# Kernel optimization log

Hardware: AMD Instinct MI355X
Metric: run time of the kernel (lower is better)

The kernel has to match this reference:

```python
import jax, jax.numpy as jnp
import numpy as np

N_NODES = 50000
N_EDGES = 800000
D = 128
N_GRAPHS = 64
EPS = 1e-5


def _bn(x, g, b):
    # BatchNorm1d training-mode statistics over the node/graph axis
    mu = x.mean(axis=0)
    var = x.var(axis=0)
    return g * (x - mu) / jnp.sqrt(var + EPS) + b


def setup_inputs() -> dict:
    key = jax.random.key(0)
    ks = jax.random.split(key, 32)
    s = 0.05
    inp = {
        'x': jax.random.normal(ks[0], (N_NODES, D), dtype=jnp.float32),
        'edge_index': jax.random.randint(ks[1], (2, N_EDGES), 0, N_NODES, dtype=jnp.int32),
        'batch': jnp.sort(jax.random.randint(ks[2], (N_NODES,), 0, N_GRAPHS, dtype=jnp.int32)),
        # stacked ResGatedGraphConv params for 3 layers (key/query/value/skip)
        'Wk': jax.random.normal(ks[3], (3, D, D)) * s,
        'bk': jnp.zeros((3, D)),
        'Wq': jax.random.normal(ks[4], (3, D, D)) * s,
        'bq': jnp.zeros((3, D)),
        'Wv': jax.random.normal(ks[5], (3, D, D)) * s,
        'bv': jnp.zeros((3, D)),
        'Ws': jax.random.normal(ks[6], (3, D, D)) * s,
        'bs': jnp.zeros((3, D)),
        # per-layer conv BatchNorm affine params
        'g_cl': jnp.ones((3, D)), 'b_cl': jnp.zeros((3, D)),
        # pool norms
        'g_gap': jnp.ones((D,)), 'b_gap': jnp.zeros((D,)),
        'g_gsp': jnp.ones((D,)), 'b_gsp': jnp.zeros((D,)),
        # MLP head: 2*D -> 256 -> 128 -> 5
        'W1': jax.random.normal(ks[7], (2 * D, 256)) * s, 'b1': jnp.zeros((256,)),
        'g1': jnp.ones((256,)), 'bt1': jnp.zeros((256,)),
        'W2': jax.random.normal(ks[8], (256, 128)) * s, 'b2': jnp.zeros((128,)),
        'g2': jnp.ones((128,)), 'bt2': jnp.zeros((128,)),
        'Wl': jax.random.normal(ks[9], (128, 5)) * s, 'bl': jnp.zeros((5,)),
    }
    return inp


def reference(x, edge_index, batch, Wk, bk, Wq, bq, Wv, bv, Ws, bs, g_cl, b_cl,
              g_gap, b_gap, g_gsp, b_gsp, W1, b1, g1, bt1, W2, b2, g2, bt2, Wl, bl):
    src, dst = edge_index[0], edge_index[1]
    n = x.shape[0]
    for i in range(3):
        k = x @ Wk[i] + bk[i]   # target-side gate term
        q = x @ Wq[i] + bq[i]   # source-side gate term
        v = x @ Wv[i] + bv[i]   # messages
        gate = jax.nn.sigmoid(k[dst] + q[src])          # [E, D]
        agg = jax.ops.segment_sum(gate * v[src], dst, num_segments=n)
        x = agg + x @ Ws[i] + bs[i]                      # residual skip
        x = jax.nn.relu(x)
        x = _bn(x, g_cl[i], b_cl[i])
        # dropout: identity in eval mode
    counts = jax.ops.segment_sum(jnp.ones((n,), x.dtype), batch, num_segments=N_GRAPHS)
    gap = jax.ops.segment_sum(x, batch, num_segments=N_GRAPHS) / jnp.maximum(counts, 1.0)[:, None]
    gsp = jax.ops.segment_max(x, batch, num_segments=N_GRAPHS)
    gsp = jnp.where(counts[:, None] > 0, gsp, 0.0)
    gap = _bn(gap, g_gap, b_gap)
    gsp = _bn(gsp, g_gsp, b_gsp)
    out = jnp.concatenate([gap, gsp], axis=1)            # [G, 2D]
    out = _bn(jax.nn.relu(out @ W1 + b1), g1, bt1)
    out = _bn(jax.nn.relu(out @ W2 + b2), g2, bt2)
    return out @ Wl + bl                                  # [G, 5]
```

## Files before the change

### kernel.cpp

```cpp
#include <hip/hip_runtime.h>
#include <math.h>

#define N_NODES 50000
#define N_PAD 50048
#define N_EDGES 800000
#define D 128
#define N_GRAPHS 64
#define EPS 1e-5f
#define PCHUNK 16
#define GSTRIPES 8
#define SCAN_NB 196

typedef __attribute__((ext_vector_type(8))) short bf16x8;
typedef __attribute__((ext_vector_type(4))) float f32x4;
typedef __attribute__((ext_vector_type(2))) _Float16 h16x2;

static inline size_t align256(size_t x) { return (x + 255) & ~(size_t)255; }

__device__ inline unsigned short f2bf(float x) {
    unsigned u = __builtin_bit_cast(unsigned, x);
    u += 0x7FFFu + ((u >> 16) & 1u);
    return (unsigned short)(u >> 16);
}
__device__ inline float bf2f(unsigned short h) {
    unsigned u = (unsigned)h << 16;
    return __builtin_bit_cast(float, u);
}
__device__ inline unsigned short f2h(float x) {
    _Float16 h = (_Float16)x;
    return __builtin_bit_cast(unsigned short, h);
}

__device__ inline float fsigmoid(float z) {
    return __builtin_amdgcn_rcpf(1.0f + __expf(-z));
}

__global__ void prep_w(const float* __restrict__ Wk, const float* __restrict__ Wq,
                       const float* __restrict__ Wv, const float* __restrict__ Ws,
                       unsigned short* __restrict__ Whi, unsigned short* __restrict__ Wlo)
{
    const int j = blockIdx.x & 127;
    const int mat = (blockIdx.x >> 7) & 3;
    const int layer = blockIdx.x >> 9;
    const int k = threadIdx.x;
    const float* Wsrc = (mat == 0) ? Wk : (mat == 1) ? Wq : (mat == 2) ? Wv : Ws;
    const float w = Wsrc[((size_t)layer * D + k) * D + j];
    const unsigned short hi = f2bf(w);
    const unsigned short lo = f2bf(w - bf2f(hi));
    const size_t o = (((size_t)layer * 4 + mat) * D + j) * D + k;
    Whi[o] = hi;
    Wlo[o] = lo;
}

__global__ void convert_split(const float* __restrict__ X,
                              unsigned short* __restrict__ Xhi, unsigned short* __restrict__ Xlo)
{
    const size_t idx = (size_t)blockIdx.x * blockDim.x + threadIdx.x;
    if (idx >= (size_t)N_PAD * (D / 4)) return;
    const size_t n = idx >> 5;
    float4 v = make_float4(0.f, 0.f, 0.f, 0.f);
    if (n < N_NODES) v = ((const float4*)X)[idx];
    float xv[4] = {v.x, v.y, v.z, v.w};
    unsigned short hi[4], lo[4];
    #pragma unroll
    for (int c = 0; c < 4; ++c) {
        hi[c] = f2bf(xv[c]);
        lo[c] = f2bf(xv[c] - bf2f(hi[c]));
    }
    ((ushort4*)Xhi)[idx] = make_ushort4(hi[0], hi[1], hi[2], hi[3]);
    ((ushort4*)Xlo)[idx] = make_ushort4(lo[0], lo[1], lo[2], lo[3]);
}

__global__ void gemm_kqvs_mfma(
    const unsigned short* __restrict__ Xhi, const unsigned short* __restrict__ Xlo,
    const unsigned short* __restrict__ Whi, const unsigned short* __restrict__ Wlo,
    const float* __restrict__ bk, const float* __restrict__ bq,
    const float* __restrict__ bv, const float* __restrict__ bs,
    float* __restrict__ Kb, unsigned short* __restrict__ QVh, float* __restrict__ Sb)
{
    const int tid = threadIdx.x;
    const int wave = tid >> 6;
    const int mat = wave >> 1;
    const int cq = (wave & 1) + 2 * blockIdx.y;
    const int lane = tid & 63;
    const int l16 = lane & 15;
    const int lhi = lane >> 4;

    const unsigned short* wh = Whi + (size_t)mat * D * D;
    const unsigned short* wl = Wlo + (size_t)mat * D * D;
    bf16x8 bh[2][4], bl[2][4];
    #pragma unroll
    for (int t2 = 0; t2 < 2; ++t2) {
        const int tc = (cq * 2 + t2) * 16 + l16;
        const size_t wb = (size_t)tc * D;
        #pragma unroll
        for (int c = 0; c < 4; ++c) {
            bh[t2][c] = *(const bf16x8*)(wh + wb + c * 32 + lhi * 8);
            bl[t2][c] = *(const bf16x8*)(wl + wb + c * 32 + lhi * 8);
        }
    }

    const float* bb = (mat == 0) ? bk : (mat == 1) ? bq : (mat == 2) ? bv : bs;
    float bias[2];
    #pragma unroll
    for (int t2 = 0; t2 < 2; ++t2) bias[t2] = bb[(cq * 2 + t2) * 16 + l16];

    for (int s = 0; s < GSTRIPES; ++s) {
        const int r0 = (blockIdx.x * GSTRIPES + s) * 16;
        bf16x8 ah[4], al[4];
        const size_t arow = (size_t)(r0 + l16) * D;
        #pragma unroll
        for (int c = 0; c < 4; ++c) {
            ah[c] = *(const bf16x8*)(Xhi + arow + c * 32 + lhi * 8);
            al[c] = *(const bf16x8*)(Xlo + arow + c * 32 + lhi * 8);
        }
        f32x4 acc[2];
        acc[0] = (f32x4){0.f, 0.f, 0.f, 0.f};
        acc[1] = (f32x4){0.f, 0.f, 0.f, 0.f};
        #pragma unroll
        for (int t2 = 0; t2 < 2; ++t2) {
            #pragma unroll
            for (int c = 0; c < 4; ++c) {
                acc[t2] = __builtin_amdgcn_mfma_f32_16x16x32_bf16(ah[c], bh[t2][c], acc[t2], 0, 0, 0);
                acc[t2] = __builtin_amdgcn_mfma_f32_16x16x32_bf16(al[c], bh[t2][c], acc[t2], 0, 0, 0);
                acc[t2] = __builtin_amdgcn_mfma_f32_16x16x32_bf16(ah[c], bl[t2][c], acc[t2], 0, 0, 0);
            }
        }
        if (mat == 0 || mat == 3) {
            float* ob = (mat == 0) ? Kb : Sb;
            #pragma unroll
            for (int t2 = 0; t2 < 2; ++t2) {
                const int lc = (cq * 2 + t2) * 16 + l16;
                #pragma unroll
                for (int rgi = 0; rgi < 4; ++rgi) {
                    const int row = r0 + lhi * 4 + rgi;
                    if (row < N_NODES) ob[(size_t)row * D + lc] = acc[t2][rgi] + bias[t2];
                }
            }
        } else {
            unsigned short* base = QVh + ((mat == 2) ? 1 : 0);
            #pragma unroll
            for (int t2 = 0; t2 < 2; ++t2) {
                const int lc = (cq * 2 + t2) * 16 + l16;
                #pragma unroll
                for (int rgi = 0; rgi < 4; ++rgi) {
                    const int row = r0 + lhi * 4 + rgi;
                    if (row < N_NODES) base[2 * ((size_t)row * D + lc)] = f2h(acc[t2][rgi] + bias[t2]);
                }
            }
        }
    }
}

__global__ void hist_dst(const int* __restrict__ dst, int* __restrict__ cnt) {
    int e = blockIdx.x * blockDim.x + threadIdx.x;
    if (e < N_EDGES) atomicAdd(&cnt[dst[e]], 1);
}

__global__ void scan_block_sums(const int* __restrict__ cnt, int* __restrict__ bsum) {
    __shared__ int s[256];
    const int t = threadIdx.x;
    const int i = blockIdx.x * 256 + t;
    s[t] = (i < N_NODES) ? cnt[i] : 0;
    __syncthreads();
    #pragma unroll
    for (int off = 128; off > 0; off >>= 1) {
        if (t < off) s[t] += s[t + off];
        __syncthreads();
    }
    if (t == 0) bsum[blockIdx.x] = s[0];
}

__global__ void scan_block_offsets(const int* __restrict__ bsum, int* __restrict__ boff) {
    __shared__ int s[256];
    const int t = threadIdx.x;
    s[t] = (t < SCAN_NB) ? bsum[t] : 0;
    __syncthreads();
    for (int off = 1; off < 256; off <<= 1) {
        const int add = (t >= off) ? s[t - off] : 0;
        __syncthreads();
        s[t] += add;
        __syncthreads();
    }
    if (t < SCAN_NB) boff[t] = (t == 0) ? 0 : s[t - 1];
}

__global__ void scan_final(const int* __restrict__ cnt, const int* __restrict__ boff,
                           int* __restrict__ row_start, int* __restrict__ cursor) {
    __shared__ int s[256];
    const int t = threadIdx.x;
    const int i = blockIdx.x * 256 + t;
    const int v = (i < N_NODES) ? cnt[i] : 0;
    s[t] = v;
    __syncthreads();
    for (int off = 1; off < 256; off <<= 1) {
        const int add = (t >= off) ? s[t - off] : 0;
        __syncthreads();
        s[t] += add;
        __syncthreads();
    }
    if (i < N_NODES) {
        const int excl = boff[blockIdx.x] + s[t] - v;
        row_start[i] = excl;
        cursor[i] = excl;
    }
    if (i == N_NODES - 1) {
        row_start[N_NODES] = N_EDGES;
        cursor[N_NODES] = N_EDGES;
    }
}

__global__ void fill_csr(const int* __restrict__ src, const int* __restrict__ dst,
                         int* __restrict__ cursor, int* __restrict__ col) {
    int e = blockIdx.x * blockDim.x + threadIdx.x;
    if (e < N_EDGES) {
        int d = dst[e];
        int p = atomicAdd(&cursor[d], 1);
        col[p] = src[e];
    }
}

__global__ void aggregate(const float* __restrict__ Kb, const unsigned int* __restrict__ QV,
                          const float* __restrict__ Sb,
                          const int* __restrict__ row_start, const int* __restrict__ col,
                          float* __restrict__ H)
{
    const int tid = threadIdx.x;
    const int node = blockIdx.x * 2 + (tid >> 7);
    const int d = tid & 127;
    const float kd = Kb[(size_t)node * D + d];
    float acc = 0.f;
    const int e0 = row_start[node];
    const int e1 = row_start[node + 1];
    int e = e0;
    for (; e + 4 <= e1; e += 4) {
        const int s0 = col[e + 0];
        const int s1 = col[e + 1];
        const int s2 = col[e + 2];
        const int s3 = col[e + 3];
        const unsigned u0 = QV[(size_t)s0 * D + d];
        const unsigned u1 = QV[(size_t)s1 * D + d];
        const unsigned u2 = QV[(size_t)s2 * D + d];
        const unsigned u3 = QV[(size_t)s3 * D + d];
        const h16x2 a0 = __builtin_bit_cast(h16x2, u0);
        const h16x2 a1 = __builtin_bit_cast(h16x2, u1);
        const h16x2 a2 = __builtin_bit_cast(h16x2, u2);
        const h16x2 a3 = __builtin_bit_cast(h16x2, u3);
        acc = fmaf(fsigmoid(kd + (float)a0[0]), (float)a0[1], acc);
        acc = fmaf(fsigmoid(kd + (float)a1[0]), (float)a1[1], acc);
        acc = fmaf(fsigmoid(kd + (float)a2[0]), (float)a2[1], acc);
        acc = fmaf(fsigmoid(kd + (float)a3[0]), (float)a3[1], acc);
    }
    for (; e < e1; ++e) {
        const int s = col[e];
        const h16x2 a = __builtin_bit_cast(h16x2, QV[(size_t)s * D + d]);
        acc = fmaf(fsigmoid(kd + (float)a[0]), (float)a[1], acc);
    }
    H[(size_t)node * D + d] = fmaxf(acc + Sb[(size_t)node * D + d], 0.0f);
}

__global__ void bn_stats(const float* __restrict__ H, float* __restrict__ fsum,
                         float* __restrict__ fsq)
{
    __shared__ float s1[256], s2[256];
    const int tid = threadIdx.x;
    const int d = tid & 127;
    const int rowoff = tid >> 7;
    float sum = 0.f, sq = 0.f;
    for (int n = blockIdx.x * 2 + rowoff; n < N_NODES; n += gridDim.x * 2) {
        const float v = H[(size_t)n * D + d];
        sum += v; sq += v * v;
    }
    s1[tid] = sum; s2[tid] = sq;
    __syncthreads();
    if (tid < 128) {
        atomicAdd(&fsum[d], s1[tid] + s1[tid + 128]);
        atomicAdd(&fsq[d],  s2[tid] + s2[tid + 128]);
    }
}

__global__ void bn_apply(float* __restrict__ H, const float* __restrict__ fsum,
                         const float* __restrict__ fsq, const float* __restrict__ g,
                         const float* __restrict__ b)
{
    const int idx = blockIdx.x * blockDim.x + threadIdx.x;
    const int total = N_NODES * D / 4;
    if (idx >= total) return;
    float4 h = ((const float4*)H)[idx];
    float hv[4] = {h.x, h.y, h.z, h.w};
    const int dbase = (idx * 4) & 127;
    float o[4];
    #pragma unroll
    for (int c = 0; c < 4; ++c) {
        const int d = dbase + c;
        const float mu = fsum[d] * (1.0f / N_NODES);
        const float var = fsq[d] * (1.0f / N_NODES) - mu * mu;
        const float sc = g[d] * rsqrtf(var + EPS);
        o[c] = (hv[c] - mu) * sc + b[d];
    }
    ((float4*)H)[idx] = make_float4(o[0], o[1], o[2], o[3]);
}

__global__ void find_gstart(const int* __restrict__ batch, int* __restrict__ gstart) {
    const int g = threadIdx.x;
    if (g > N_GRAPHS) return;
    int lo = 0, hi = N_NODES;
    while (lo < hi) {
        int mid = (lo + hi) >> 1;
        if (batch[mid] < g) lo = mid + 1; else hi = mid;
    }
    gstart[g] = lo;
}

__global__ void pool_partial(const float* __restrict__ X, const int* __restrict__ gstart,
                             float* __restrict__ psum, float* __restrict__ pmax)
{
    const int g = blockIdx.x / PCHUNK;
    const int c = blockIdx.x % PCHUNK;
    const int d = threadIdx.x;
    const int lo = gstart[g], hi = gstart[g + 1];
    float sum = 0.f, mx = -INFINITY;
    for (int n = lo + c; n < hi; n += PCHUNK) {
        const float v = X[(size_t)n * D + d];
        sum += v;
        mx = fmaxf(mx, v);
    }
    psum[(size_t)blockIdx.x * D + d] = sum;
    pmax[(size_t)blockIdx.x * D + d] = mx;
}

__global__ void pool_combine(const float* __restrict__ psum, const float* __restrict__ pmax,
                             const int* __restrict__ gstart,
                             float* __restrict__ gap, float* __restrict__ gsp)
{
    const int g = blockIdx.x;
    const int d = threadIdx.x;
    float sum = 0.f, mx = -INFINITY;
    #pragma unroll
    for (int c = 0; c < PCHUNK; ++c) {
        sum += psum[(size_t)(g * PCHUNK + c) * D + d];
        mx = fmaxf(mx, pmax[(size_t)(g * PCHUNK + c) * D + d]);
    }
    const int cnt = gstart[g + 1] - gstart[g];
    gap[g * D + d] = sum / fmaxf((float)cnt, 1.0f);
    gsp[g * D + d] = (cnt > 0) ? mx : 0.0f;
}

__global__ void bn_rows(const float* __restrict__ A, int rows, int cols,
                        const float* __restrict__ g, const float* __restrict__ b,
                        float* __restrict__ out, int out_cols, int out_off)
{
    const int c = blockIdx.x * blockDim.x + threadIdx.x;
    if (c >= cols) return;
    float sum = 0.f, sq = 0.f;
    for (int r = 0; r < rows; ++r) {
        const float v = A[r * cols + c];
        sum += v; sq += v * v;
    }
    const float mu = sum / rows;
    const float var = sq / rows - mu * mu;
    const float sc = g[c] * rsqrtf(var + EPS);
    const float sh = b[c] - mu * sc;
    for (int r = 0; r < rows; ++r) {
        out[r * out_cols + out_off + c] = A[r * cols + c] * sc + sh;
    }
}

__global__ void gemm_small(const float* __restrict__ A, const float* __restrict__ W,
                           const float* __restrict__ bias, float* __restrict__ out,
                           int K, int C, int relu)
{
    __shared__ float as[256];
    const int r = blockIdx.x;
    for (int k = threadIdx.x; k < K; k += blockDim.x) as[k] = A[r * K + k];
    __syncthreads();
    const int j = threadIdx.x;
    if (j < C) {
        float acc = bias[j];
        for (int k = 0; k < K; ++k) acc = fmaf(as[k], W[k * C + j], acc);
        if (relu) acc = fmaxf(acc, 0.f);
        out[r * C + j] = acc;
    }
}

extern "C" void kernel_launch(void* const* d_in, const int* in_sizes, int n_in,
                              void* d_out, int out_size, void* d_ws, size_t ws_size,
                              hipStream_t stream)
{
    const float* x     = (const float*)d_in[0];
    const int*   ei    = (const int*)d_in[1];
    const int*   srcE  = ei;
    const int*   dstE  = ei + N_EDGES;
    const int*   batch = (const int*)d_in[2];
    const float* Wk = (const float*)d_in[3];  const float* bk = (const float*)d_in[4];
    const float* Wq = (const float*)d_in[5];  const float* bq = (const float*)d_in[6];
    const float* Wv = (const float*)d_in[7];  const float* bv = (const float*)d_in[8];
    const float* Ws = (const float*)d_in[9];  const float* bs = (const float*)d_in[10];
    const float* g_cl = (const float*)d_in[11]; const float* b_cl = (const float*)d_in[12];
    const float* g_gap = (const float*)d_in[13]; const float* b_gap = (const float*)d_in[14];
    const float* g_gsp = (const float*)d_in[15]; const float* b_gsp = (const float*)d_in[16];
    const float* W1 = (const float*)d_in[17]; const float* b1 = (const float*)d_in[18];
    const float* g1 = (const float*)d_in[19]; const float* bt1 = (const float*)d_in[20];
    const float* W2 = (const float*)d_in[21]; const float* b2 = (const float*)d_in[22];
    const float* g2 = (const float*)d_in[23]; const float* bt2 = (const float*)d_in[24];
    const float* Wl = (const float*)d_in[25]; const float* bl = (const float*)d_in[26];
    float* out = (float*)d_out;

    char* ws = (char*)d_ws;
    size_t off = 0;
    const size_t bufB = (size_t)N_NODES * D * sizeof(float);
    float* Kb = (float*)(ws + off); off = align256(off + bufB);
    unsigned short* QVh = (unsigned short*)(ws + off); off = align256(off + bufB);
    float* Sb = (float*)(ws + off); off = align256(off + bufB);
    float* H  = (float*)(ws + off); off = align256(off + bufB);
    unsigned short* Xhi = (unsigned short*)(ws + off); off = align256(off + (size_t)N_PAD * D * 2);
    unsigned short* Xlo = (unsigned short*)(ws + off); off = align256(off + (size_t)N_PAD * D * 2);
    unsigned short* Whi = (unsigned short*)(ws + off); off = align256(off + (size_t)12 * D * D * 2);
    unsigned short* Wlo = (unsigned short*)(ws + off); off = align256(off + (size_t)12 * D * D * 2);
    float* fsum = (float*)(ws + off); off = align256(off + 128 * sizeof(float));
    float* fsq  = (float*)(ws + off); off = align256(off + 128 * sizeof(float));
    int* cnt       = (int*)(ws + off); off = align256(off + (size_t)N_NODES * sizeof(int));
    int* row_start = (int*)(ws + off); off = align256(off + (size_t)(N_NODES + 1) * sizeof(int));
    int* cursor    = (int*)(ws + off); off = align256(off + (size_t)(N_NODES + 1) * sizeof(int));
    int* colI      = (int*)(ws + off); off = align256(off + (size_t)N_EDGES * sizeof(int));
    int* bsum      = (int*)(ws + off); off = align256(off + 256 * sizeof(int));
    int* boff      = (int*)(ws + off); off = align256(off + 256 * sizeof(int));
    int* gstart    = (int*)(ws + off); off = align256(off + (N_GRAPHS + 1) * sizeof(int));
    float* psum = (float*)(ws + off); off = align256(off + (size_t)N_GRAPHS * PCHUNK * D * sizeof(float));
    float* pmax = (float*)(ws + off); off = align256(off + (size_t)N_GRAPHS * PCHUNK * D * sizeof(float));
    float* gap = (float*)(ws + off); off = align256(off + (size_t)N_GRAPHS * D * sizeof(float));
    float* gsp = (float*)(ws + off); off = align256(off + (size_t)N_GRAPHS * D * sizeof(float));
    float* h0  = (float*)(ws + off); off = align256(off + (size_t)N_GRAPHS * 256 * sizeof(float));
    float* h1  = (float*)(ws + off); off = align256(off + (size_t)N_GRAPHS * 256 * sizeof(float));
    float* h2  = (float*)(ws + off); off = align256(off + (size_t)N_GRAPHS * 128 * sizeof(float));
    if (off > ws_size) return;

    hipMemsetAsync(cnt, 0, (size_t)N_NODES * sizeof(int), stream);
    hist_dst<<<(N_EDGES + 255) / 256, 256, 0, stream>>>(dstE, cnt);
    scan_block_sums<<<SCAN_NB, 256, 0, stream>>>(cnt, bsum);
    scan_block_offsets<<<1, 256, 0, stream>>>(bsum, boff);
    scan_final<<<SCAN_NB, 256, 0, stream>>>(cnt, boff, row_start, cursor);
    fill_csr<<<(N_EDGES + 255) / 256, 256, 0, stream>>>(srcE, dstE, cursor, colI);
    find_gstart<<<1, 128, 0, stream>>>(batch, gstart);
    prep_w<<<12 * 128, 128, 0, stream>>>(Wk, Wq, Wv, Ws, Whi, Wlo);
    convert_split<<<(N_PAD * (D / 4) + 255) / 256, 256, 0, stream>>>(x, Xhi, Xlo);

    for (int i = 0; i < 3; ++i) {
        gemm_kqvs_mfma<<<dim3(N_PAD / (16 * GSTRIPES), 2), 512, 0, stream>>>(
            Xhi, Xlo,
            Whi + (size_t)i * 4 * D * D, Wlo + (size_t)i * 4 * D * D,
            bk + i * D, bq + i * D, bv + i * D, bs + i * D,
            Kb, QVh, Sb);
        aggregate<<<N_NODES / 2, 256, 0, stream>>>(Kb, (const unsigned int*)QVh, Sb, row_start, colI, H);
        hipMemsetAsync(fsum, 0, 128 * sizeof(float), stream);
        hipMemsetAsync(fsq, 0, 128 * sizeof(float), stream);
        bn_stats<<<256, 256, 0, stream>>>(H, fsum, fsq);
        bn_apply<<<(N_NODES * D / 4 + 255) / 256, 256, 0, stream>>>(
            H, fsum, fsq, g_cl + i * D, b_cl + i * D);
        if (i < 2) {
            convert_split<<<(N_PAD * (D / 4) + 255) / 256, 256, 0, stream>>>(H, Xhi, Xlo);
        }
    }

    pool_partial<<<N_GRAPHS * PCHUNK, 128, 0, stream>>>(H, gstart, psum, pmax);
    pool_combine<<<N_GRAPHS, 128, 0, stream>>>(psum, pmax, gstart, gap, gsp);
    bn_rows<<<1, 128, 0, stream>>>(gap, N_GRAPHS, 128, g_gap, b_gap, h0, 256, 0);
    bn_rows<<<1, 128, 0, stream>>>(gsp, N_GRAPHS, 128, g_gsp, b_gsp, h0, 256, 128);

    gemm_small<<<N_GRAPHS, 256, 0, stream>>>(h0, W1, b1, h1, 256, 256, 1);
    bn_rows<<<1, 256, 0, stream>>>(h1, N_GRAPHS, 256, g1, bt1, h1, 256, 0);
    gemm_small<<<N_GRAPHS, 256, 0, stream>>>(h1, W2, b2, h2, 256, 128, 1);
    bn_rows<<<1, 128, 0, stream>>>(h2, N_GRAPHS, 128, g2, bt2, h2, 128, 0);
    gemm_small<<<N_GRAPHS, 256, 0, stream>>>(h2, Wl, bl, out, 128, 5, 0);
}
```

Measured before the change: 869.2 us.

## Stage GEMM weight fragments in LDS with narrower column tiles per block

Restructures the KQVS GEMM so each 256-thread block handles a single 16-column slice for all four matrices, one wave per matrix. The block first stages the hi/lo weight fragments into shared memory and reads them back per MFMA step, instead of each wave holding two column tiles of weights in registers. The grid grows from 2 to 8 column groups, which cuts register pressure and raises block count. In exchange, the A-row fragments (Xhi/Xlo) are reloaded by four times as many blocks, and there are extra LDS reads inside the inner loop.

```diff
diff --git a/kernel.cpp b/kernel.cpp
--- a/kernel.cpp
+++ b/kernel.cpp
@@ -78,32 +78,30 @@
     const float* __restrict__ bv, const float* __restrict__ bs,
     float* __restrict__ Kb, unsigned short* __restrict__ QVh, float* __restrict__ Sb)
 {
+    __shared__ short lbh[4][4][64][8];
+    __shared__ short lbl[4][4][64][8];
+
     const int tid = threadIdx.x;
     const int wave = tid >> 6;
-    const int mat = wave >> 1;
-    const int cq = (wave & 1) + 2 * blockIdx.y;
     const int lane = tid & 63;
     const int l16 = lane & 15;
     const int lhi = lane >> 4;
-
-    const unsigned short* wh = Whi + (size_t)mat * D * D;
-    const unsigned short* wl = Wlo + (size_t)mat * D * D;
-    bf16x8 bh[2][4], bl[2][4];
-    #pragma unroll
-    for (int t2 = 0; t2 < 2; ++t2) {
-        const int tc = (cq * 2 + t2) * 16 + l16;
-        const size_t wb = (size_t)tc * D;
-        #pragma unroll
-        for (int c = 0; c < 4; ++c) {
-            bh[t2][c] = *(const bf16x8*)(wh + wb + c * 32 + lhi * 8);
-            bl[t2][c] = *(const bf16x8*)(wl + wb + c * 32 + lhi * 8);
-        }
-    }
-
-    const float* bb = (mat == 0) ? bk : (mat == 1) ? bq : (mat == 2) ? bv : bs;
-    float bias[2];
-    #pragma unroll
-    for (int t2 = 0; t2 < 2; ++t2) bias[t2] = bb[(cq * 2 + t2) * 16 + l16];
+    const int colbase = blockIdx.y * 16;
+
+    for (int i = tid; i < 4 * 4 * 64; i += 256) {
+        const int m = i >> 8;
+        const int cc = (i >> 6) & 3;
+        const int ln = i & 63;
+        const int col = colbase + (ln & 15);
+        const int koff = cc * 32 + (ln >> 4) * 8;
+        const size_t src = ((size_t)m * D + col) * D + koff;
+        *(bf16x8*)&lbh[m][cc][ln][0] = *(const bf16x8*)(Whi + src);
+        *(bf16x8*)&lbl[m][cc][ln][0] = *(const bf16x8*)(Wlo + src);
+    }
+    __syncthreads();
+
+    const float* bb = (wave == 0) ? bk : (wave == 1) ? bq : (wave == 2) ? bv : bs;
+    const float bias = bb[colbase + l16];
 
     for (int s = 0; s < GSTRIPES; ++s) {
         const int r0 = (blockIdx.x * GSTRIPES + s) * 16;
@@ -114,39 +112,29 @@
             ah[c] = *(const bf16x8*)(Xhi + arow + c * 32 + lhi * 8);
             al[c] = *(const bf16x8*)(Xlo + arow + c * 32 + lhi * 8);
         }
-        f32x4 acc[2];
-        acc[0] = (f32x4){0.f, 0.f, 0.f, 0.f};
-        acc[1] = (f32x4){0.f, 0.f, 0.f, 0.f};
+        f32x4 acc = (f32x4){0.f, 0.f, 0.f, 0.f};
         #pragma unroll
-        for (int t2 = 0; t2 < 2; ++t2) {
+        for (int c = 0; c < 4; ++c) {
+            const bf16x8 bh = *(const bf16x8*)&lbh[wave][c][lane][0];
+            const bf16x8 bl = *(const bf16x8*)&lbl[wave][c][lane][0];
+            acc = __builtin_amdgcn_mfma_f32_16x16x32_bf16(ah[c], bh, acc, 0, 0, 0);
+            acc = __builtin_amdgcn_mfma_f32_16x16x32_bf16(al[c], bh, acc, 0, 0, 0);
+            acc = __builtin_amdgcn_mfma_f32_16x16x32_bf16(ah[c], bl, acc, 0, 0, 0);
+        }
+        const int lc = colbase + l16;
+        if (wave == 0 || wave == 3) {
+            float* ob = (wave == 0) ? Kb : Sb;
             #pragma unroll
-            for (int c = 0; c < 4; ++c) {
-                acc[t2] = __builtin_amdgcn_mfma_f32_16x16x32_bf16(ah[c], bh[t2][c], acc[t2], 0, 0, 0);
-                acc[t2] = __builtin_amdgcn_mfma_f32_16x16x32_bf16(al[c], bh[t2][c], acc[t2], 0, 0, 0);
-                acc[t2] = __builtin_amdgcn_mfma_f32_16x16x32_bf16(ah[c], bl[t2][c], acc[t2], 0, 0, 0);
-            }
-        }
-        if (mat == 0 || mat == 3) {
-            float* ob = (mat == 0) ? Kb : Sb;
-            #pragma unroll
-            for (int t2 = 0; t2 < 2; ++t2) {
-                const int lc = (cq * 2 + t2) * 16 + l16;
-                #pragma unroll
-                for (int rgi = 0; rgi < 4; ++rgi) {
-                    const int row = r0 + lhi * 4 + rgi;
-                    if (row < N_NODES) ob[(size_t)row * D + lc] = acc[t2][rgi] + bias[t2];
-                }
+            for (int rgi = 0; rgi < 4; ++rgi) {
+                const int row = r0 + lhi * 4 + rgi;
+                if (row < N_NODES) ob[(size_t)row * D + lc] = acc[rgi] + bias;
             }
         } else {
-            unsigned short* base = QVh + ((mat == 2) ? 1 : 0);
+            unsigned short* base = QVh + ((wave == 2) ? 1 : 0);
             #pragma unroll
-            for (int t2 = 0; t2 < 2; ++t2) {
-                const int lc = (cq * 2 + t2) * 16 + l16;
-                #pragma unroll
-                for (int rgi = 0; rgi < 4; ++rgi) {
-                    const int row = r0 + lhi * 4 + rgi;
-                    if (row < N_NODES) base[2 * ((size_t)row * D + lc)] = f2h(acc[t2][rgi] + bias[t2]);
-                }
+            for (int rgi = 0; rgi < 4; ++rgi) {
+                const int row = r0 + lhi * 4 + rgi;
+                if (row < N_NODES) base[2 * ((size_t)row * D + lc)] = f2h(acc[rgi] + bias);
             }
         }
     }
@@ -446,7 +434,7 @@
     convert_split<<<(N_PAD * (D / 4) + 255) / 256, 256, 0, stream>>>(x, Xhi, Xlo);
 
     for (int i = 0; i < 3; ++i) {
-        gemm_kqvs_mfma<<<dim3(N_PAD / (16 * GSTRIPES), 2), 512, 0, stream>>>(
+        gemm_kqvs_mfma<<<dim3(N_PAD / (16 * GSTRIPES), 8), 256, 0, stream>>>(
             Xhi, Xlo,
             Whi + (size_t)i * 4 * D * D, Wlo + (size_t)i * 4 * D * D,
             bk + i * D, bq + i * D, bv + i * D, bs + i * D,
```

After: 979.7 us. 1.13x slower.
